# Kernel tuning notes

Hardware: AMD Instinct MI355X
Metric: run time of the kernel (lower is better)

## Reference

```python
import jax, jax.numpy as jnp
import numpy as np

EPS = 1e-5  # PyTorch BatchNorm1d default eps


def setup_inputs() -> dict:
    key = jax.random.key(0)
    ks = jax.random.split(key, 16)
    M, B, S, H = 2, 4, 2048, 4096
    HID, INT = 256, 128  # head_hidden_dim, head_hidden_dim // 2
    randn = lambda k, shape, scale=1.0: jax.random.normal(k, shape, jnp.float32) * scale
    return {
        'h': randn(ks[0], (M, B, S, H)),
        'w1': randn(ks[1], (M, HID, H), 0.02),
        'b1': randn(ks[2], (M, HID), 0.02),
        'g1': jax.random.uniform(ks[3], (M, HID), jnp.float32, 0.5, 1.5),
        'be1': randn(ks[4], (M, HID), 0.02),
        'm1': randn(ks[5], (M, HID), 0.1),
        'v1': jax.random.uniform(ks[6], (M, HID), jnp.float32, 0.5, 1.5),
        'w2': randn(ks[7], (M, INT, HID), 0.05),
        'b2': randn(ks[8], (M, INT), 0.02),
        'g2': jax.random.uniform(ks[9], (M, INT), jnp.float32, 0.5, 1.5),
        'be2': randn(ks[10], (M, INT), 0.02),
        'm2': randn(ks[11], (M, INT), 0.1),
        'v2': jax.random.uniform(ks[12], (M, INT), jnp.float32, 0.5, 1.5),
        'w3': randn(ks[13], (M, 1, INT), 0.05),
        'b3': randn(ks[14], (M, 1), 0.02),
    }


def _bn_eval(x, gamma, beta, mean, var):
    # eval-mode BatchNorm1d over the feature axis; per-model params broadcast
    # x: [M,B,S,K]; params: [M,K]
    inv = gamma * jax.lax.rsqrt(var + EPS)  # [M,K]
    return x * inv[:, None, None, :] + (beta - mean * inv)[:, None, None, :]


def reference(h, w1, b1, g1, be1, m1, v1, w2, b2, g2, be2, m2, v2, w3, b3):
    # Vectorized equivalent of the per-position Python loop applying each
    # model's ScalarProjectionHead to every token representation.
    x = jnp.einsum('mbsh,mkh->mbsk', h, w1) + b1[:, None, None, :]   # [M,B,S,256]
    x = jax.nn.relu(_bn_eval(x, g1, be1, m1, v1))                     # dropout = identity (eval)
    x = jnp.einsum('mbsk,mjk->mbsj', x, w2) + b2[:, None, None, :]   # [M,B,S,128]
    x = jax.nn.relu(_bn_eval(x, g2, be2, m2, v2))
    s = jnp.einsum('mbsj,moj->mbso', x, w3) + b3[:, None, None, :]   # [M,B,S,1]
    # stack per-model scores along last dim, as torch.stack(..., dim=-1)
    all_raw_scores = jnp.transpose(s[..., 0], (1, 2, 0))             # [B,S,M]
    return all_raw_scores
```

## Files before the change

kernel.cpp:

```cpp
#include <hip/hip_runtime.h>
#include <hip/hip_bf16.h>

#define EPSF 1e-5f

typedef __attribute__((ext_vector_type(8))) short bf16x8;
typedef __attribute__((ext_vector_type(4))) float f32x4;
typedef __attribute__((ext_vector_type(4))) unsigned int u32x4;

__device__ __forceinline__ unsigned short f2bf(float f) {
  union { float f; unsigned u; } v; v.f = f;
  unsigned r = v.u + 0x7fffu + ((v.u >> 16) & 1u);
  return (unsigned short)(r >> 16);
}

__device__ __forceinline__ u32x4 cvtpk8(f32x4 a, f32x4 b) {
  u32x4 r;
  asm("v_cvt_pk_bf16_f32 %0, %1, %2" : "=v"(r[0]) : "v"(a[0]), "v"(a[1]));
  asm("v_cvt_pk_bf16_f32 %0, %1, %2" : "=v"(r[1]) : "v"(a[2]), "v"(a[3]));
  asm("v_cvt_pk_bf16_f32 %0, %1, %2" : "=v"(r[2]) : "v"(b[0]), "v"(b[1]));
  asm("v_cvt_pk_bf16_f32 %0, %1, %2" : "=v"(r[3]) : "v"(b[2]), "v"(b[3]));
  return r;
}

__global__ void prep_kernel(const float* __restrict__ w1, const float* __restrict__ b1,
                            const float* __restrict__ g1, const float* __restrict__ be1,
                            const float* __restrict__ m1, const float* __restrict__ v1,
                            const float* __restrict__ w2, const float* __restrict__ b2,
                            const float* __restrict__ g2, const float* __restrict__ be2,
                            const float* __restrict__ m2, const float* __restrict__ v2,
                            unsigned short* __restrict__ w1p, unsigned short* __restrict__ w2f,
                            float* __restrict__ bias1, float* __restrict__ bias2) {
  int idx = blockIdx.x * blockDim.x + threadIdx.x;
  int stride = gridDim.x * blockDim.x;
  for (int i = idx; i < 262144; i += stride) {
    int l  = i & 63;
    int f  = (i >> 6) & 7;
    int kt = (i >> 9) & 63;
    int c  = (i >> 15) & 3;
    int m  = i >> 17;
    int st = f >> 2, j = f & 3;
    int n  = c * 64 + j * 16 + (l & 15);
    int k0 = kt * 64 + st * 32 + (l >> 4) * 8;
    int mn = m * 256 + n;
    float inv = g1[mn] * rsqrtf(v1[mn] + EPSF);
    const float* src = w1 + (size_t)mn * 4096 + k0;
    unsigned short* dst = w1p + (size_t)i * 8;
#pragma unroll
    for (int e = 0; e < 8; ++e) dst[e] = f2bf(src[e] * inv);
  }
  for (int i = idx; i < 2 * 128 * 256; i += stride) {
    int mj = i >> 8;
    float inv = g2[mj] * rsqrtf(v2[mj] + EPSF);
    w2f[i] = f2bf(w2[i] * inv);
  }
  if (idx < 512) {
    float inv = g1[idx] * rsqrtf(v1[idx] + EPSF);
    bias1[idx] = b1[idx] * inv + be1[idx] - m1[idx] * inv;
  }
  if (idx < 256) {
    float inv = g2[idx] * rsqrtf(v2[idx] + EPSF);
    bias2[idx] = b2[idx] * inv + be2[idx] - m2[idx] * inv;
  }
}

#define BLOAD(BN, KT)                                                  \
  {                                                                    \
    BN[0] = *(const bf16x8*)(pB + (size_t)(KT) * 8192 + 0);            \
    BN[1] = *(const bf16x8*)(pB + (size_t)(KT) * 8192 + 1024);         \
    BN[2] = *(const bf16x8*)(pB + (size_t)(KT) * 8192 + 4096);         \
    BN[3] = *(const bf16x8*)(pB + (size_t)(KT) * 8192 + 5120);         \
  }

#define ALOAD(AR, KOFF)                                                \
  {                                                                    \
    AR[0] = *(const f32x4*)(aSrc + (KOFF));                            \
    AR[1] = *(const f32x4*)(aSrc + (KOFF) + 4);                        \
  }

#define AWRITE(AR, DBASE)                                              \
  {                                                                    \
    u32x4 w_ = cvtpk8(AR[0], AR[1]);                                   \
    *(u32x4*)((DBASE) + aOff) = w_;                                    \
  }

#define AFREAD(ABUF)                                                   \
  {                                                                    \
    _Pragma("unroll") for (int st = 0; st < 2; ++st)                   \
    _Pragma("unroll") for (int i = 0; i < 4; ++i) {                    \
      int row_ = i * 16 + l15;                                         \
      int g_ = st * 4 + lq;                                            \
      aF[st][i] = *(const bf16x8*)((ABUF) + row_ * 128 + ((g_ ^ (row_ & 7)) << 4)); \
    }                                                                  \
  }

#define MFMA8(BC)                                                      \
  {                                                                    \
    _Pragma("unroll") for (int st = 0; st < 2; ++st)                   \
    _Pragma("unroll") for (int i = 0; i < 4; ++i)                      \
    _Pragma("unroll") for (int j = 0; j < 2; ++j)                      \
      acc[i][j] = __builtin_amdgcn_mfma_f32_16x16x32_bf16(aF[st][i], BC[st * 2 + j], acc[i][j], 0, 0, 0); \
  }

#define BOUNDARY()                                                     \
  __builtin_amdgcn_sched_barrier(0x77);                                \
  asm volatile("s_waitcnt lgkmcnt(0)");                                \
  __builtin_amdgcn_s_barrier();                                        \
  __builtin_amdgcn_sched_barrier(0x77);

__global__ __launch_bounds__(512) void fused_heads_kernel(
    const float* __restrict__ h,
    const unsigned short* __restrict__ w1p,
    const unsigned short* __restrict__ w2f,
    const float* __restrict__ bias1,
    const float* __restrict__ bias2,
    const float* __restrict__ w3,
    const float* __restrict__ b3,
    float* __restrict__ out) {
  __shared__ __align__(16) char lds[34816];

  const int tid = threadIdx.x;
  const int lane = tid & 63;
  const int wv = tid >> 6;
  const int l15 = lane & 15;
  const int lq = lane >> 4;

  const int bid = blockIdx.x;
  const int mdl = (bid >> 2) & 1;
  const int rb = (bid >> 3) * 4 + (bid & 3);

  const float* hM = h + ((size_t)mdl * 8192 + (size_t)rb * 64) * 4096;
  const char* pB = (const char*)w1p + (size_t)(mdl * 4 + (wv >> 1)) * 524288
                   + (wv & 1) * 2048 + lane * 16;

  const int arow = tid >> 3;
  const int akseg = tid & 7;
  const float* aSrc = hM + (size_t)arow * 4096 + akseg * 8;
  const int aOff = arow * 128 + ((akseg ^ (arow & 7)) << 4);

  f32x4 acc[4][2];
#pragma unroll
  for (int i = 0; i < 4; ++i)
#pragma unroll
    for (int j = 0; j < 2; ++j)
#pragma unroll
      for (int q = 0; q < 4; ++q) acc[i][j][q] = 0.f;

  bf16x8 bb0[4], bb1[4];
  f32x4 aR0[2], aR1[2];
  bf16x8 aF[2][4];

  char* const Ab0 = lds;
  char* const Ab1 = lds + 8192;

  ALOAD(aR0, 0)
  BLOAD(bb0, 0)
  ALOAD(aR1, 64)
  AWRITE(aR0, Ab0)
  BOUNDARY()

#pragma unroll 1
  for (int kt2 = 0; kt2 < 31; ++kt2) {
    const int kt = kt2 * 2;
    AFREAD(Ab0)
    BLOAD(bb1, kt + 1)
    ALOAD(aR0, (kt + 2) * 64)
    MFMA8(bb0)
    AWRITE(aR1, Ab1)
    BOUNDARY()
    AFREAD(Ab1)
    BLOAD(bb0, kt + 2)
    ALOAD(aR1, (kt + 3) * 64)
    MFMA8(bb1)
    AWRITE(aR0, Ab0)
    BOUNDARY()
  }
  AFREAD(Ab0)
  BLOAD(bb1, 63)
  MFMA8(bb0)
  AWRITE(aR1, Ab1)
  BOUNDARY()
  AFREAD(Ab1)
  MFMA8(bb1)
  BOUNDARY()

  float b1v[2];
#pragma unroll
  for (int j = 0; j < 2; ++j) b1v[j] = bias1[mdl * 256 + wv * 32 + j * 16 + l15];
#pragma unroll
  for (int i = 0; i < 4; ++i) {
#pragma unroll
    for (int j = 0; j < 2; ++j) {
      int n = wv * 32 + j * 16 + l15;
#pragma unroll
      for (int q = 0; q < 4; ++q) {
        int row = i * 16 + lq * 4 + q;
        float x = fmaxf(acc[i][j][q] + b1v[j], 0.f);
        *(unsigned short*)(lds + row * 512 + ((((n >> 3) ^ (row & 7)) << 4) | ((n & 7) << 1))) = f2bf(x);
      }
    }
  }
  __syncthreads();

  f32x4 acc2[4];
#pragma unroll
  for (int i = 0; i < 4; ++i)
#pragma unroll
    for (int q = 0; q < 4; ++q) acc2[i][q] = 0.f;

  const unsigned short* w2m = w2f + mdl * (128 * 256);
#pragma unroll
  for (int st = 0; st < 8; ++st) {
    int k8 = st * 32 + lq * 8;
    bf16x8 aX[4], bW;
#pragma unroll
    for (int i = 0; i < 4; ++i) {
      int row = i * 16 + l15;
      aX[i] = *(const bf16x8*)(lds + row * 512 + ((((k8 >> 3) ^ (row & 7)) << 4)));
    }
    {
      int n2 = wv * 16 + l15;
      bW = *(const bf16x8*)(w2m + n2 * 256 + k8);
    }
#pragma unroll
    for (int i = 0; i < 4; ++i)
      acc2[i] = __builtin_amdgcn_mfma_f32_16x16x32_bf16(aX[i], bW, acc2[i], 0, 0, 0);
  }

  float w3v, b2v;
  {
    int n2 = wv * 16 + l15;
    w3v = w3[mdl * 128 + n2];
    b2v = bias2[mdl * 128 + n2];
  }
  float* part = (float*)(lds + 32768);
#pragma unroll
  for (int i = 0; i < 4; ++i) {
#pragma unroll
    for (int q = 0; q < 4; ++q) {
      float x = fmaxf(acc2[i][q] + b2v, 0.f);
      float val = x * w3v;
#pragma unroll
      for (int mk = 1; mk < 16; mk <<= 1) val += __shfl_xor(val, mk, 64);
      if (l15 == 0) part[wv * 64 + i * 16 + lq * 4 + q] = val;
    }
  }
  __syncthreads();
  if (tid < 64) {
    float s = part[tid] + part[64 + tid] + part[128 + tid] + part[192 + tid]
            + part[256 + tid] + part[320 + tid] + part[384 + tid] + part[448 + tid]
            + b3[mdl];
    out[((size_t)(rb * 64 + tid)) * 2 + mdl] = s;
  }
}

extern "C" void kernel_launch(void* const* d_in, const int* in_sizes, int n_in,
                              void* d_out, int out_size, void* d_ws, size_t ws_size,
                              hipStream_t stream) {
  const float* h   = (const float*)d_in[0];
  const float* w1  = (const float*)d_in[1];
  const float* b1  = (const float*)d_in[2];
  const float* g1  = (const float*)d_in[3];
  const float* be1 = (const float*)d_in[4];
  const float* m1  = (const float*)d_in[5];
  const float* v1  = (const float*)d_in[6];
  const float* w2  = (const float*)d_in[7];
  const float* b2  = (const float*)d_in[8];
  const float* g2  = (const float*)d_in[9];
  const float* be2 = (const float*)d_in[10];
  const float* m2  = (const float*)d_in[11];
  const float* v2  = (const float*)d_in[12];
  const float* w3  = (const float*)d_in[13];
  const float* b3  = (const float*)d_in[14];

  char* ws = (char*)d_ws;
  unsigned short* w1p = (unsigned short*)ws;
  unsigned short* w2f = (unsigned short*)(ws + 4194304);
  float* bias1 = (float*)(ws + 4325376);
  float* bias2 = (float*)(ws + 4327424);

  prep_kernel<<<1024, 256, 0, stream>>>(w1, b1, g1, be1, m1, v1,
                                        w2, b2, g2, be2, m2, v2,
                                        w1p, w2f, bias1, bias2);
  fused_heads_kernel<<<256, 512, 0, stream>>>(h, w1p, w2f, bias1, bias2, w3, b3,
                                              (float*)d_out);
}
```

Before: 72.40 us.

## Double the K-step per pipeline stage to halve barriers in first GEMM

```diff
diff --git a/kernel.cpp b/kernel.cpp
--- a/kernel.cpp
+++ b/kernel.cpp
@@ -63,49 +63,62 @@
   }
 }
 
-#define BLOAD(BN, KT)                                                  \
-  {                                                                    \
-    BN[0] = *(const bf16x8*)(pB + (size_t)(KT) * 8192 + 0);            \
-    BN[1] = *(const bf16x8*)(pB + (size_t)(KT) * 8192 + 1024);         \
-    BN[2] = *(const bf16x8*)(pB + (size_t)(KT) * 8192 + 4096);         \
-    BN[3] = *(const bf16x8*)(pB + (size_t)(KT) * 8192 + 5120);         \
-  }
-
-#define ALOAD(AR, KOFF)                                                \
-  {                                                                    \
-    AR[0] = *(const f32x4*)(aSrc + (KOFF));                            \
-    AR[1] = *(const f32x4*)(aSrc + (KOFF) + 4);                        \
-  }
-
-#define AWRITE(AR, DBASE)                                              \
-  {                                                                    \
-    u32x4 w_ = cvtpk8(AR[0], AR[1]);                                   \
-    *(u32x4*)((DBASE) + aOff) = w_;                                    \
-  }
-
-#define AFREAD(ABUF)                                                   \
-  {                                                                    \
-    _Pragma("unroll") for (int st = 0; st < 2; ++st)                   \
-    _Pragma("unroll") for (int i = 0; i < 4; ++i) {                    \
-      int row_ = i * 16 + l15;                                         \
-      int g_ = st * 4 + lq;                                            \
-      aF[st][i] = *(const bf16x8*)((ABUF) + row_ * 128 + ((g_ ^ (row_ & 7)) << 4)); \
-    }                                                                  \
-  }
-
-#define MFMA8(BC)                                                      \
-  {                                                                    \
-    _Pragma("unroll") for (int st = 0; st < 2; ++st)                   \
-    _Pragma("unroll") for (int i = 0; i < 4; ++i)                      \
-    _Pragma("unroll") for (int j = 0; j < 2; ++j)                      \
-      acc[i][j] = __builtin_amdgcn_mfma_f32_16x16x32_bf16(aF[st][i], BC[st * 2 + j], acc[i][j], 0, 0, 0); \
-  }
-
-#define BOUNDARY()                                                     \
-  __builtin_amdgcn_sched_barrier(0x77);                                \
-  asm volatile("s_waitcnt lgkmcnt(0)");                                \
-  __builtin_amdgcn_s_barrier();                                        \
+#define BLOAD8(BN, T)                                                   \
+  {                                                                     \
+    BN[0] = *(const bf16x8*)(pB + (size_t)(2*(T)) * 8192 + 0);          \
+    BN[1] = *(const bf16x8*)(pB + (size_t)(2*(T)) * 8192 + 1024);       \
+    BN[2] = *(const bf16x8*)(pB + (size_t)(2*(T)) * 8192 + 4096);       \
+    BN[3] = *(const bf16x8*)(pB + (size_t)(2*(T)) * 8192 + 5120);       \
+    BN[4] = *(const bf16x8*)(pB + (size_t)(2*(T)+1) * 8192 + 0);        \
+    BN[5] = *(const bf16x8*)(pB + (size_t)(2*(T)+1) * 8192 + 1024);     \
+    BN[6] = *(const bf16x8*)(pB + (size_t)(2*(T)+1) * 8192 + 4096);     \
+    BN[7] = *(const bf16x8*)(pB + (size_t)(2*(T)+1) * 8192 + 5120);     \
+  }
+
+#define ALOAD4(AR, T)                                                   \
+  {                                                                     \
+    AR[0] = *(const f32x4*)(aSrc + (T) * 128);                          \
+    AR[1] = *(const f32x4*)(aSrc + (T) * 128 + 4);                      \
+    AR[2] = *(const f32x4*)(aSrc + (T) * 128 + 8);                      \
+    AR[3] = *(const f32x4*)(aSrc + (T) * 128 + 12);                     \
+  }
+
+#define AWRITE2(AR, DBASE)                                              \
+  {                                                                     \
+    u32x4 lo_ = cvtpk8(AR[0], AR[1]);                                   \
+    u32x4 hi_ = cvtpk8(AR[2], AR[3]);                                   \
+    *(u32x4*)((DBASE) + aOff0) = lo_;                                   \
+    *(u32x4*)((DBASE) + aOff1) = hi_;                                   \
+  }
+
+#define AMM_ST(ST, ABUF, BC)                                            \
+  {                                                                     \
+    _Pragma("unroll") for (int i = 0; i < 4; ++i) {                     \
+      int row_ = i * 16 + l15;                                          \
+      int g_ = (ST) * 4 + lq;                                           \
+      aF[i] = *(const bf16x8*)((ABUF) + row_ * 256 + ((g_ ^ (row_ & 15)) << 4)); \
+    }                                                                   \
+    _Pragma("unroll") for (int i = 0; i < 4; ++i)                       \
+    _Pragma("unroll") for (int j = 0; j < 2; ++j)                       \
+      acc[i][j] = __builtin_amdgcn_mfma_f32_16x16x32_bf16(               \
+          aF[i], BC[((ST) >> 1) * 4 + ((ST) & 1) * 2 + j], acc[i][j], 0, 0, 0); \
+  }
+
+#define BOUNDARY()                                                      \
+  __builtin_amdgcn_sched_barrier(0x77);                                 \
+  asm volatile("s_waitcnt lgkmcnt(0)");                                 \
+  __builtin_amdgcn_s_barrier();                                         \
   __builtin_amdgcn_sched_barrier(0x77);
+
+#define INTERVAL_FULL(T, BC, BN, ARL, ARW, ABR, ABW)                    \
+  BLOAD8(BN, (T) + 1)                                                   \
+  ALOAD4(ARL, (T) + 2)                                                  \
+  AWRITE2(ARW, ABW)                                                     \
+  AMM_ST(0, ABR, BC)                                                    \
+  AMM_ST(1, ABR, BC)                                                    \
+  AMM_ST(2, ABR, BC)                                                    \
+  AMM_ST(3, ABR, BC)                                                    \
+  BOUNDARY()
 
 __global__ __launch_bounds__(512) void fused_heads_kernel(
     const float* __restrict__ h,
@@ -133,9 +146,10 @@
                    + (wv & 1) * 2048 + lane * 16;
 
   const int arow = tid >> 3;
-  const int akseg = tid & 7;
-  const float* aSrc = hM + (size_t)arow * 4096 + akseg * 8;
-  const int aOff = arow * 128 + ((akseg ^ (arow & 7)) << 4);
+  const int aseg = tid & 7;
+  const float* aSrc = hM + (size_t)arow * 4096 + aseg * 16;
+  const int aOff0 = arow * 256 + ((((aseg * 2)     ) ^ (arow & 15)) << 4);
+  const int aOff1 = arow * 256 + ((((aseg * 2) + 1 ) ^ (arow & 15)) << 4);
 
   f32x4 acc[4][2];
 #pragma unroll
@@ -145,42 +159,35 @@
 #pragma unroll
       for (int q = 0; q < 4; ++q) acc[i][j][q] = 0.f;
 
-  bf16x8 bb0[4], bb1[4];
-  f32x4 aR0[2], aR1[2];
-  bf16x8 aF[2][4];
+  bf16x8 b0[8], b1[8];
+  f32x4 aRa[4], aRb[4];
+  bf16x8 aF[4];
 
   char* const Ab0 = lds;
-  char* const Ab1 = lds + 8192;
-
-  ALOAD(aR0, 0)
-  BLOAD(bb0, 0)
-  ALOAD(aR1, 64)
-  AWRITE(aR0, Ab0)
+  char* const Ab1 = lds + 16384;
+
+  ALOAD4(aRa, 0)
+  BLOAD8(b0, 0)
+  ALOAD4(aRb, 1)
+  AWRITE2(aRa, Ab0)
   BOUNDARY()
 
 #pragma unroll 1
-  for (int kt2 = 0; kt2 < 31; ++kt2) {
-    const int kt = kt2 * 2;
-    AFREAD(Ab0)
-    BLOAD(bb1, kt + 1)
-    ALOAD(aR0, (kt + 2) * 64)
-    MFMA8(bb0)
-    AWRITE(aR1, Ab1)
-    BOUNDARY()
-    AFREAD(Ab1)
-    BLOAD(bb0, kt + 2)
-    ALOAD(aR1, (kt + 3) * 64)
-    MFMA8(bb1)
-    AWRITE(aR0, Ab0)
-    BOUNDARY()
-  }
-  AFREAD(Ab0)
-  BLOAD(bb1, 63)
-  MFMA8(bb0)
-  AWRITE(aR1, Ab1)
-  BOUNDARY()
-  AFREAD(Ab1)
-  MFMA8(bb1)
+  for (int t2 = 0; t2 < 15; ++t2) {
+    INTERVAL_FULL(2 * t2,     b0, b1, aRa, aRb, Ab0, Ab1)
+    INTERVAL_FULL(2 * t2 + 1, b1, b0, aRb, aRa, Ab1, Ab0)
+  }
+  BLOAD8(b1, 31)
+  AWRITE2(aRb, Ab1)
+  AMM_ST(0, Ab0, b0)
+  AMM_ST(1, Ab0, b0)
+  AMM_ST(2, Ab0, b0)
+  AMM_ST(3, Ab0, b0)
+  BOUNDARY()
+  AMM_ST(0, Ab1, b1)
+  AMM_ST(1, Ab1, b1)
+  AMM_ST(2, Ab1, b1)
+  AMM_ST(3, Ab1, b1)
   BOUNDARY()
 
   float b1v[2];
```

Result: slower. 75.13 us (+3.8%).
